# Optimization experiments

Measured on AMD Instinct MI355X. Metric: run time of the kernel, lower is better.

## Reference

```python
import jax, jax.numpy as jnp
import numpy as np

EMBED_DIM = 256
NUM_EMBEDDINGS = 1024
COMMITMENT_COST = 0.25


def setup_inputs() -> dict:
    key = jax.random.key(0)
    k1, k2 = jax.random.split(key)
    z_e = jax.random.normal(k1, (64, 32, 32, EMBED_DIM), dtype=jnp.float32)
    # variance_scaling(fan_in, uniform) ~ U(-sqrt(3/fan_in), sqrt(3/fan_in))
    lim = float(np.sqrt(3.0 / EMBED_DIM))
    codebook = jax.random.uniform(k2, (NUM_EMBEDDINGS, EMBED_DIM), dtype=jnp.float32,
                                  minval=-lim, maxval=lim)
    return {"z_e": z_e, "codebook": codebook}


def reference(z_e, codebook):
    codebook = jnp.asarray(codebook, dtype=jnp.float32)
    z_flat = jnp.reshape(z_e, (-1, codebook.shape[1]))  # [N, D]
    # ||z||^2 - 2 z.c + ||c||^2 -> [N, K]
    distances = (jnp.sum(z_flat ** 2, axis=1, keepdims=True)
                 - 2.0 * jnp.dot(z_flat, codebook.T)
                 + jnp.sum(codebook ** 2, axis=1))
    encoding_indices = jnp.argmin(distances, axis=1)  # [N]
    quantized = jnp.reshape(codebook[encoding_indices], z_e.shape)
    commitment_loss = COMMITMENT_COST * jnp.mean((jax.lax.stop_gradient(quantized) - z_e) ** 2)
    embedding_loss = jnp.mean((quantized - jax.lax.stop_gradient(z_e)) ** 2)
    quantized = z_e + jax.lax.stop_gradient(quantized - z_e)  # straight-through
    return (quantized, commitment_loss, embedding_loss, encoding_indices)
```

## Files before the change

kernel.cpp:

```cpp
#include <hip/hip_runtime.h>

#define NROWS  65536
#define DIM    256
#define KCB    1024
#define DELTA  0.012f
#define DELTA2 2.0e-4f

typedef __attribute__((ext_vector_type(8))) _Float16 v8h;
typedef __attribute__((ext_vector_type(4))) float v4f;
typedef __attribute__((ext_vector_type(4))) int   v4i;

__device__ __forceinline__ unsigned short h16(float x) {
  _Float16 h = (_Float16)x;
  return __builtin_bit_cast(unsigned short, h);
}
__device__ __forceinline__ unsigned pk2h(float a, float b) {
  return (unsigned)h16(a) | ((unsigned)h16(b) << 16);
}
__device__ __forceinline__ v4i pk8h(float4 a, float4 b) {
  v4i r; r.x = (int)pk2h(a.x,a.y); r.y = (int)pk2h(a.z,a.w);
  r.z = (int)pk2h(b.x,b.y); r.w = (int)pk2h(b.z,b.w);
  return r;
}
__device__ __forceinline__ float f16f(float x) { return (float)(_Float16)x; }
__device__ __forceinline__ void gld16(const void* g, void* l) {
  __builtin_amdgcn_global_load_lds(
      (const __attribute__((address_space(1))) unsigned int*)g,
      (__attribute__((address_space(3))) unsigned int*)l, 16, 0, 0);
}

__global__ __launch_bounds__(256) void prep_kernel(const float* __restrict__ cb,
                                                   float* __restrict__ cnorm,
                                                   unsigned short* __restrict__ cbh,
                                                   unsigned short* __restrict__ cbl,
                                                   int* __restrict__ cnt,
                                                   int* __restrict__ cnt2) {
  int g = blockIdx.x * 256 + threadIdx.x;
  if (g == 0) { *cnt = 0; *cnt2 = 0; }
  int k = g >> 2, q = g & 3;
  int nt = k >> 7, c = k & 127;
  const float4* row = reinterpret_cast<const float4*>(cb + (size_t)k * DIM) + q * 16;
  size_t off = (size_t)((nt * 4 + q) * 128 + c) * 64;
  unsigned short* dh = cbh + off;
  unsigned short* dl = cbl + off;
  int xr = (c & 7) << 3;
  double s = 0.0;
#pragma unroll
  for (int i = 0; i < 8; ++i) {
    float4 a = row[2 * i], b = row[2 * i + 1];
    s += (double)a.x * a.x + (double)a.y * a.y + (double)a.z * a.z + (double)a.w * a.w;
    s += (double)b.x * b.x + (double)b.y * b.y + (double)b.z * b.z + (double)b.w * b.w;
    *(v4i*)(dh + ((i * 8) ^ xr)) = pk8h(a, b);
    float4 ar, br;
    ar.x = a.x - f16f(a.x); ar.y = a.y - f16f(a.y);
    ar.z = a.z - f16f(a.z); ar.w = a.w - f16f(a.w);
    br.x = b.x - f16f(b.x); br.y = b.y - f16f(b.y);
    br.z = b.z - f16f(b.z); br.w = b.w - f16f(b.w);
    *(v4i*)(dl + ((i * 8) ^ xr)) = pk8h(ar, br);
  }
  s += __shfl_xor(s, 1);
  s += __shfl_xor(s, 2);
  if (q == 0) cnorm[k] = (float)s;
}

__global__ __launch_bounds__(256, 2) void vq_mfma(
    const float* __restrict__ z, const unsigned short* __restrict__ cbh,
    const float* __restrict__ cnw, int* __restrict__ idx_arr,
    int* __restrict__ list, int* __restrict__ cnt) {
  __shared__ __align__(16) short S[32768];

  const int t = threadIdx.x;
  const int l = t & 63;
  const int w = t >> 6;
  const int l15 = l & 15, lhi = l >> 4;
  const int wm = w * 32;
  const int r0 = blockIdx.x * 128;

#pragma unroll
  for (int p = 0; p < 16; ++p) {
    int u = t + p * 256;
    int row = u >> 5, k8 = u & 31;
    const float4* s = (const float4*)(z + (size_t)(r0 + row) * DIM + k8 * 8);
    float4 a = s[0], b = s[1];
    *(v4i*)(S + row * 256 + ((k8 * 8) ^ ((row & 7) << 3))) = pk8h(a, b);
  }
  __syncthreads();

  v8h A[2][8];
#pragma unroll
  for (int mf = 0; mf < 2; ++mf) {
    int arow = wm + mf * 16 + l15;
    int base = arow * 256, xr = (arow & 7) << 3;
#pragma unroll
    for (int ks8 = 0; ks8 < 8; ++ks8)
      A[mf][ks8] = *(const v8h*)(S + base + ((ks8 * 32 + lhi * 8) ^ xr));
  }
  __syncthreads();

  auto stageC = [&](int p) {
    const char* gb = (const char*)cbh + (size_t)p * 32768 + w * 8192 + l * 16;
    char* lb = (char*)(S + (p & 1) * 16384) + w * 8192;
#pragma unroll
    for (int j = 0; j < 8; ++j) gld16(gb + j * 1024, lb + j * 1024);
  };

  int bcode[8], boff[8], bxr[8];
#pragma unroll
  for (int nf = 0; nf < 8; ++nf) {
    bcode[nf] = nf * 16 + l15;
    boff[nf] = bcode[nf] * 64;
    bxr[nf] = (bcode[nf] & 7) << 3;
  }

  float m1[8], m2[8]; int i1[8];
#pragma unroll
  for (int sl = 0; sl < 8; ++sl) { m1[sl] = 3.0e38f; m2[sl] = 3.0e38f; i1[sl] = 0; }

  stageC(0);
  __syncthreads();

  for (int nt = 0; nt < 8; ++nt) {
    float cnv[8];
#pragma unroll
    for (int nf = 0; nf < 8; ++nf) cnv[nf] = cnw[nt * 128 + bcode[nf]];

    v4f acc[2][8];
#pragma unroll
    for (int mf = 0; mf < 2; ++mf)
#pragma unroll
      for (int nf = 0; nf < 8; ++nf) acc[mf][nf] = (v4f){0.f, 0.f, 0.f, 0.f};

    for (int kh = 0; kh < 2; ++kh) {
      int p = nt * 2 + kh;
      if (p < 15) stageC(p + 1);
      const short* cur = S + (p & 1) * 16384;
#pragma unroll
      for (int ks = 0; ks < 4; ++ks) {
        int sub = (ks >> 1) * 8192;
        int ko = (ks & 1) * 32 + lhi * 8;
        v8h b[8];
#pragma unroll
        for (int nf = 0; nf < 8; ++nf)
          b[nf] = *(const v8h*)(cur + sub + boff[nf] + (ko ^ bxr[nf]));
#pragma unroll
        for (int mf = 0; mf < 2; ++mf)
#pragma unroll
          for (int nf = 0; nf < 8; ++nf)
            acc[mf][nf] = __builtin_amdgcn_mfma_f32_16x16x32_f16(A[mf][kh * 4 + ks], b[nf], acc[mf][nf], 0, 0, 0);
      }
      __syncthreads();
    }

#pragma unroll
    for (int mf = 0; mf < 2; ++mf)
#pragma unroll
      for (int nf = 0; nf < 8; ++nf) {
        int code = nt * 128 + bcode[nf];
#pragma unroll
        for (int r = 0; r < 4; ++r) {
          float s = fmaf(-2.f, acc[mf][nf][r], cnv[nf]);
          int sl = mf * 4 + r;
          m2[sl] = fminf(m2[sl], fmaxf(m1[sl], s));
          bool lt = s < m1[sl];
          i1[sl] = lt ? code : i1[sl];
          m1[sl] = lt ? s : m1[sl];
        }
      }
  }

#pragma unroll
  for (int off = 1; off < 16; off <<= 1) {
#pragma unroll
    for (int sl = 0; sl < 8; ++sl) {
      float o1 = __shfl_xor(m1[sl], off);
      int   oi = __shfl_xor(i1[sl], off);
      float o2 = __shfl_xor(m2[sl], off);
      bool bb = (o1 < m1[sl]) || (o1 == m1[sl] && oi < i1[sl]);
      float hi = fmaxf(m1[sl], o1);
      m2[sl] = fminf(hi, fminf(m2[sl], o2));
      m1[sl] = bb ? o1 : m1[sl];
      i1[sl] = bb ? oi : i1[sl];
    }
  }

  if (l15 == 0) {
#pragma unroll
    for (int sl = 0; sl < 8; ++sl) {
      int row = wm + (sl >> 2) * 16 + lhi * 4 + (sl & 3);
      idx_arr[r0 + row] = i1[sl];
      if (m2[sl] - m1[sl] < DELTA) {
        int p = atomicAdd(cnt, 1);
        list[p] = r0 + row;
      }
    }
  }
}

__global__ __launch_bounds__(256, 2) void vq_refine(
    const float* __restrict__ z,
    const unsigned short* __restrict__ cbh, const unsigned short* __restrict__ cbl,
    const float* __restrict__ cnw, const int* __restrict__ list,
    const int* __restrict__ cnt, int* __restrict__ idx_arr,
    int* __restrict__ list2, int* __restrict__ cnt2) {
  __shared__ __align__(16) short Ch[2][128 * 64];
  __shared__ __align__(16) short Cl[2][128 * 64];
  __shared__ int rows_s[64];

  const int t = threadIdx.x;
  const int l = t & 63, w = t >> 6;
  const int l15 = l & 15, lhi = l >> 4;
  const int n = *cnt;
  const int ngroups = (n + 63) >> 6;

  auto stage2 = [&](int g, int buf) {
    size_t go = (size_t)g * 16384 + w * 4096 + l * 16;
    char* lh = (char*)Ch[buf] + w * 4096;
    char* ll = (char*)Cl[buf] + w * 4096;
#pragma unroll
    for (int j = 0; j < 4; ++j) gld16((const char*)cbh + go + j * 1024, lh + j * 1024);
#pragma unroll
    for (int j = 0; j < 4; ++j) gld16((const char*)cbl + go + j * 1024, ll + j * 1024);
  };

  const int bxr = (l15 & 7) << 3;

  for (int grp = blockIdx.x; grp < ngroups; grp += gridDim.x) {
    int base = grp * 64;
    __syncthreads();
    if (t < 64) rows_s[t] = list[min(base + t, n - 1)];
    __syncthreads();
    int rowg = rows_s[w * 16 + l15];

    v8h Ah[8], Al[8];
#pragma unroll
    for (int ks8 = 0; ks8 < 8; ++ks8) {
      const float* p = z + (size_t)rowg * 256 + ks8 * 32 + lhi * 8;
      float4 a = *(const float4*)p, b = *(const float4*)(p + 4);
      v8h hv, lv;
      hv[0] = (_Float16)a.x; lv[0] = (_Float16)(a.x - (float)hv[0]);
      hv[1] = (_Float16)a.y; lv[1] = (_Float16)(a.y - (float)hv[1]);
      hv[2] = (_Float16)a.z; lv[2] = (_Float16)(a.z - (float)hv[2]);
      hv[3] = (_Float16)a.w; lv[3] = (_Float16)(a.w - (float)hv[3]);
      hv[4] = (_Float16)b.x; lv[4] = (_Float16)(b.x - (float)hv[4]);
      hv[5] = (_Float16)b.y; lv[5] = (_Float16)(b.y - (float)hv[5]);
      hv[6] = (_Float16)b.z; lv[6] = (_Float16)(b.z - (float)hv[6]);
      hv[7] = (_Float16)b.w; lv[7] = (_Float16)(b.w - (float)hv[7]);
      Ah[ks8] = hv; Al[ks8] = lv;
    }

    stage2(0, 0);
    __syncthreads();

    float m1[4], m2[4]; int i1[4];
#pragma unroll
    for (int r = 0; r < 4; ++r) { m1[r] = 3.0e38f; m2[r] = 3.0e38f; i1[r] = 0; }

    for (int nt = 0; nt < 8; ++nt) {
      float cnv[8];
#pragma unroll
      for (int nf = 0; nf < 8; ++nf) cnv[nf] = cnw[nt * 128 + nf * 16 + l15];

      v4f acc[8];
#pragma unroll
      for (int nf = 0; nf < 8; ++nf) acc[nf] = (v4f){0.f, 0.f, 0.f, 0.f};

      for (int kc = 0; kc < 4; ++kc) {
        int g = nt * 4 + kc;
        if (g < 31) stage2(g + 1, (g + 1) & 1);
        const short* ch = Ch[g & 1];
        const short* cl = Cl[g & 1];
#pragma unroll
        for (int ks = 0; ks < 2; ++ks) {
          int ko = (ks * 32 + lhi * 8) ^ bxr;
          v8h bh[8], bl[8];
#pragma unroll
          for (int nf = 0; nf < 8; ++nf) {
            int bo = (nf * 16 + l15) * 64 + ko;
            bh[nf] = *(const v8h*)(ch + bo);
            bl[nf] = *(const v8h*)(cl + bo);
          }
          v8h ah = Ah[kc * 2 + ks], al = Al[kc * 2 + ks];
#pragma unroll
          for (int nf = 0; nf < 8; ++nf) {
            acc[nf] = __builtin_amdgcn_mfma_f32_16x16x32_f16(al, bh[nf], acc[nf], 0, 0, 0);
            acc[nf] = __builtin_amdgcn_mfma_f32_16x16x32_f16(ah, bl[nf], acc[nf], 0, 0, 0);
            acc[nf] = __builtin_amdgcn_mfma_f32_16x16x32_f16(ah, bh[nf], acc[nf], 0, 0, 0);
          }
        }
        __syncthreads();
      }

#pragma unroll
      for (int nf = 0; nf < 8; ++nf) {
        int code = nt * 128 + nf * 16 + l15;
#pragma unroll
        for (int r = 0; r < 4; ++r) {
          float s = fmaf(-2.f, acc[nf][r], cnv[nf]);
          m2[r] = fminf(m2[r], fmaxf(m1[r], s));
          bool lt = s < m1[r];
          i1[r] = lt ? code : i1[r];
          m1[r] = lt ? s : m1[r];
        }
      }
    }

#pragma unroll
    for (int off = 1; off < 16; off <<= 1) {
#pragma unroll
      for (int r = 0; r < 4; ++r) {
        float o1 = __shfl_xor(m1[r], off);
        int   oi = __shfl_xor(i1[r], off);
        float o2 = __shfl_xor(m2[r], off);
        bool bb = (o1 < m1[r]) || (o1 == m1[r] && oi < i1[r]);
        float hi = fmaxf(m1[r], o1);
        m2[r] = fminf(hi, fminf(m2[r], o2));
        m1[r] = bb ? o1 : m1[r];
        i1[r] = bb ? oi : i1[r];
      }
    }

    if (l15 == 0) {
#pragma unroll
      for (int r = 0; r < 4; ++r) {
        int fr = w * 16 + lhi * 4 + r;
        if (base + fr < n) {
          int grow = rows_s[fr];
          idx_arr[grow] = i1[r];
          if (m2[r] - m1[r] < DELTA2) {
            int p = atomicAdd(cnt2, 1);
            list2[p] = grow;
          }
        }
      }
    }
  }
}

__global__ __launch_bounds__(256) void vq_rescue(
    const float* __restrict__ z, const float* __restrict__ cb,
    const float* __restrict__ cnw, const int* __restrict__ list,
    const int* __restrict__ cnt, int* __restrict__ idx_arr) {
  __shared__ float zs[256];
  __shared__ float As;
  __shared__ float wmin[4];
  __shared__ int   widx[4];

  const int t = threadIdx.x;
  const int l = t & 63, w = t >> 6;
  const int n = *cnt;

  for (int i = blockIdx.x; i < n; i += gridDim.x) {
    int row = list[i];
    __syncthreads();
    if (t < 64) ((float4*)zs)[t] = ((const float4*)(z + (size_t)row * DIM))[t];
    __syncthreads();
    if (t < 4) {
      double s = 0.0;
      const float* zz = zs + t * 64;
      for (int d = 0; d < 64; ++d) { float v = zz[d]; s += (double)v * v; }
      s += __shfl_xor(s, 1);
      s += __shfl_xor(s, 2);
      if (t == 0) As = (float)s;
    }
    __syncthreads();
    float Af = As;

    const float4* c0 = (const float4*)(cb + (size_t)(t      ) * DIM);
    const float4* c1 = (const float4*)(cb + (size_t)(t + 256) * DIM);
    const float4* c2 = (const float4*)(cb + (size_t)(t + 512) * DIM);
    const float4* c3 = (const float4*)(cb + (size_t)(t + 768) * DIM);
    float a0 = 0.f, a1 = 0.f, a2 = 0.f, a3 = 0.f;
    for (int d4 = 0; d4 < 64; ++d4) {
      float4 zq = *(const float4*)(zs + d4 * 4);
      float4 va = c0[d4], vb = c1[d4], vc = c2[d4], vd = c3[d4];
      a0 = fmaf(zq.x, va.x, a0); a0 = fmaf(zq.y, va.y, a0);
      a0 = fmaf(zq.z, va.z, a0); a0 = fmaf(zq.w, va.w, a0);
      a1 = fmaf(zq.x, vb.x, a1); a1 = fmaf(zq.y, vb.y, a1);
      a1 = fmaf(zq.z, vb.z, a1); a1 = fmaf(zq.w, vb.w, a1);
      a2 = fmaf(zq.x, vc.x, a2); a2 = fmaf(zq.y, vc.y, a2);
      a2 = fmaf(zq.z, vc.z, a2); a2 = fmaf(zq.w, vc.w, a2);
      a3 = fmaf(zq.x, vd.x, a3); a3 = fmaf(zq.y, vd.y, a3);
      a3 = fmaf(zq.z, vd.z, a3); a3 = fmaf(zq.w, vd.w, a3);
    }
    float accs[4] = {a0, a1, a2, a3};
    float mv = 3.0e38f; int mi = 0;
#pragma unroll
    for (int j = 0; j < 4; ++j) {
      int code = t + j * 256;
      float t1 = fmaf(-2.f, accs[j], Af);
      float t2 = t1 + cnw[code];
      if (t2 < mv) { mv = t2; mi = code; }
    }
#pragma unroll
    for (int off = 1; off < 64; off <<= 1) {
      float ov = __shfl_xor(mv, off);
      int   oi = __shfl_xor(mi, off);
      if (ov < mv || (ov == mv && oi < mi)) { mv = ov; mi = oi; }
    }
    if (l == 0) { wmin[w] = mv; widx[w] = mi; }
    __syncthreads();
    if (t == 0) {
      float bm = wmin[0]; int bi = widx[0];
#pragma unroll
      for (int q = 1; q < 4; ++q)
        if (wmin[q] < bm || (wmin[q] == bm && widx[q] < bi)) { bm = wmin[q]; bi = widx[q]; }
      idx_arr[row] = bi;
    }
    __syncthreads();
  }
}

__global__ __launch_bounds__(256) void vq_epilogue(
    const float* __restrict__ z, const float* __restrict__ cb,
    const int* __restrict__ idx_arr, float* __restrict__ out_q,
    float* __restrict__ out_idx, double* __restrict__ partial) {
  __shared__ int idxs[16];
  __shared__ double lw[4];
  const int t = threadIdx.x;
  const int b0 = blockIdx.x * 16;
  if (t < 16) {
    int k = idx_arr[b0 + t];
    idxs[t] = k;
    out_idx[b0 + t] = (float)k;
  }
  __syncthreads();
  const float4* zb = (const float4*)(z + (size_t)b0 * DIM);
  float4* qb = (float4*)(out_q + (size_t)b0 * DIM);
  double ls = 0.0;
#pragma unroll
  for (int p = 0; p < 4; ++p) {
    int fi = p * 256 + t;
    int ki = idxs[fi >> 6];
    float4 zv = zb[fi];
    float4 cv = ((const float4*)(cb + (size_t)ki * DIM))[fi & 63];
    float dx = cv.x - zv.x, dy = cv.y - zv.y, dz = cv.z - zv.z, dw = cv.w - zv.w;
    float4 o; o.x = zv.x + dx; o.y = zv.y + dy; o.z = zv.z + dz; o.w = zv.w + dw;
    qb[fi] = o;
    ls += (double)dx * dx + (double)dy * dy + (double)dz * dz + (double)dw * dw;
  }
#pragma unroll
  for (int off = 1; off < 64; off <<= 1) ls += __shfl_xor(ls, off);
  if ((t & 63) == 0) lw[t >> 6] = ls;
  __syncthreads();
  if (t == 0) partial[blockIdx.x] = lw[0] + lw[1] + lw[2] + lw[3];
}

__global__ __launch_bounds__(256) void finalize_kernel(const double* __restrict__ partial,
                                                       float* __restrict__ out_losses) {
  __shared__ double lw[4];
  const int t = threadIdx.x;
  double s = 0.0;
  for (int i = t; i < 4096; i += 256) s += partial[i];
#pragma unroll
  for (int off = 1; off < 64; off <<= 1) s += __shfl_xor(s, off);
  if ((t & 63) == 0) lw[t >> 6] = s;
  __syncthreads();
  if (t == 0) {
    double mse = (lw[0] + lw[1] + lw[2] + lw[3]) / ((double)NROWS * (double)DIM);
    out_losses[0] = (float)(0.25 * mse);
    out_losses[1] = (float)mse;
  }
}

extern "C" void kernel_launch(void* const* d_in, const int* in_sizes, int n_in,
                              void* d_out, int out_size, void* d_ws, size_t ws_size,
                              hipStream_t stream) {
  const float* z  = (const float*)d_in[0];
  const float* cb = (const float*)d_in[1];
  float* out = (float*)d_out;

  char* ws = (char*)d_ws;
  int*            cnt     = (int*)(ws + 0);
  int*            cnt2    = (int*)(ws + 8);
  float*          cnorm   = (float*)(ws + 4096);
  double*         partial = (double*)(ws + 8192);
  int*            idx_arr = (int*)(ws + 40960);
  int*            list    = (int*)(ws + 303104);
  int*            list2   = (int*)(ws + 565248);
  unsigned short* cbh     = (unsigned short*)(ws + 827392);
  unsigned short* cbl     = (unsigned short*)(ws + 1351680);

  float* out_q      = out;
  float* out_losses = out + 16777216;
  float* out_idx    = out + 16777218;

  prep_kernel<<<16, 256, 0, stream>>>(cb, cnorm, cbh, cbl, cnt, cnt2);
  vq_mfma<<<NROWS / 128, 256, 0, stream>>>(z, cbh, cnorm, idx_arr, list, cnt);
  vq_refine<<<256, 256, 0, stream>>>(z, cbh, cbl, cnorm, list, cnt, idx_arr, list2, cnt2);
  vq_rescue<<<256, 256, 0, stream>>>(z, cb, cnorm, list2, cnt2, idx_arr);
  vq_epilogue<<<NROWS / 16, 256, 0, stream>>>(z, cb, idx_arr, out_q, out_idx, partial);
  finalize_kernel<<<1, 256, 0, stream>>>(partial, out_losses);
}
```

Baseline: 170.2 us.

## Fuse epilogue into MFMA kernel, triple-buffer codebook staging, patch refined rows

Measured after the change: 324.2 us. +90.4%, slower.

```diff
diff --git a/kernel.cpp b/kernel.cpp
--- a/kernel.cpp
+++ b/kernel.cpp
@@ -65,13 +65,16 @@
 
 __global__ __launch_bounds__(256, 2) void vq_mfma(
     const float* __restrict__ z, const unsigned short* __restrict__ cbh,
-    const float* __restrict__ cnw, int* __restrict__ idx_arr,
-    int* __restrict__ list, int* __restrict__ cnt) {
+    const float* __restrict__ cnw, const float* __restrict__ cb,
+    int* __restrict__ idx_arr, int* __restrict__ list, int* __restrict__ cnt,
+    float* __restrict__ out_q, float* __restrict__ out_idx,
+    float* __restrict__ rowloss) {
   __shared__ __align__(16) short S[32768];
+  __shared__ float CNS[1024];
+  __shared__ int idxs2[128];
 
   const int t = threadIdx.x;
-  const int l = t & 63;
-  const int w = t >> 6;
+  const int l = t & 63, w = t >> 6;
   const int l15 = l & 15, lhi = l >> 4;
   const int wm = w * 32;
   const int r0 = blockIdx.x * 128;
@@ -84,6 +87,8 @@
     float4 a = s[0], b = s[1];
     *(v4i*)(S + row * 256 + ((k8 * 8) ^ ((row & 7) << 3))) = pk8h(a, b);
   }
+#pragma unroll
+  for (int j = 0; j < 4; ++j) CNS[t + j * 256] = cnw[t + j * 256];
   __syncthreads();
 
   v8h A[2][8];
@@ -97,11 +102,11 @@
   }
   __syncthreads();
 
-  auto stageC = [&](int p) {
-    const char* gb = (const char*)cbh + (size_t)p * 32768 + w * 8192 + l * 16;
-    char* lb = (char*)(S + (p & 1) * 16384) + w * 8192;
-#pragma unroll
-    for (int j = 0; j < 8; ++j) gld16(gb + j * 1024, lb + j * 1024);
+  auto stageC = [&](int g) {
+    const char* gb = (const char*)cbh + (size_t)g * 16384 + w * 4096 + l * 16;
+    char* lb = (char*)S + (g % 3) * 16384 + w * 4096 + l * 16;
+#pragma unroll
+    for (int j = 0; j < 4; ++j) gld16(gb + j * 1024, lb + j * 1024);
   };
 
   int bcode[8], boff[8], bxr[8];
@@ -116,56 +121,54 @@
 #pragma unroll
   for (int sl = 0; sl < 8; ++sl) { m1[sl] = 3.0e38f; m2[sl] = 3.0e38f; i1[sl] = 0; }
 
-  stageC(0);
-  __syncthreads();
-
-  for (int nt = 0; nt < 8; ++nt) {
-    float cnv[8];
-#pragma unroll
-    for (int nf = 0; nf < 8; ++nf) cnv[nf] = cnw[nt * 128 + bcode[nf]];
-
-    v4f acc[2][8];
-#pragma unroll
-    for (int mf = 0; mf < 2; ++mf)
-#pragma unroll
-      for (int nf = 0; nf < 8; ++nf) acc[mf][nf] = (v4f){0.f, 0.f, 0.f, 0.f};
-
-    for (int kh = 0; kh < 2; ++kh) {
-      int p = nt * 2 + kh;
-      if (p < 15) stageC(p + 1);
-      const short* cur = S + (p & 1) * 16384;
-#pragma unroll
-      for (int ks = 0; ks < 4; ++ks) {
-        int sub = (ks >> 1) * 8192;
-        int ko = (ks & 1) * 32 + lhi * 8;
-        v8h b[8];
+  v4f acc[2][8];
+
+  stageC(0); stageC(1);
+  for (int g = 0; g < 32; ++g) {
+    if (g < 31) asm volatile("s_waitcnt vmcnt(4)" ::: "memory");
+    else        asm volatile("s_waitcnt vmcnt(0)" ::: "memory");
+    __builtin_amdgcn_s_barrier();
+    __builtin_amdgcn_sched_barrier(0);
+    if (g + 2 < 32) stageC(g + 2);
+    const int kc = g & 3;
+    if (kc == 0) {
+#pragma unroll
+      for (int mf = 0; mf < 2; ++mf)
+#pragma unroll
+        for (int nf = 0; nf < 8; ++nf) acc[mf][nf] = (v4f){0.f, 0.f, 0.f, 0.f};
+    }
+    const short* cur = S + (g % 3) * 8192;
+#pragma unroll
+    for (int ks = 0; ks < 2; ++ks) {
+      v8h b[8];
+#pragma unroll
+      for (int nf = 0; nf < 8; ++nf)
+        b[nf] = *(const v8h*)(cur + boff[nf] + ((ks * 32 + lhi * 8) ^ bxr[nf]));
+#pragma unroll
+      for (int mf = 0; mf < 2; ++mf)
 #pragma unroll
         for (int nf = 0; nf < 8; ++nf)
-          b[nf] = *(const v8h*)(cur + sub + boff[nf] + (ko ^ bxr[nf]));
-#pragma unroll
-        for (int mf = 0; mf < 2; ++mf)
-#pragma unroll
-          for (int nf = 0; nf < 8; ++nf)
-            acc[mf][nf] = __builtin_amdgcn_mfma_f32_16x16x32_f16(A[mf][kh * 4 + ks], b[nf], acc[mf][nf], 0, 0, 0);
-      }
-      __syncthreads();
-    }
-
-#pragma unroll
-    for (int mf = 0; mf < 2; ++mf)
-#pragma unroll
-      for (int nf = 0; nf < 8; ++nf) {
-        int code = nt * 128 + bcode[nf];
-#pragma unroll
-        for (int r = 0; r < 4; ++r) {
-          float s = fmaf(-2.f, acc[mf][nf][r], cnv[nf]);
-          int sl = mf * 4 + r;
-          m2[sl] = fminf(m2[sl], fmaxf(m1[sl], s));
-          bool lt = s < m1[sl];
-          i1[sl] = lt ? code : i1[sl];
-          m1[sl] = lt ? s : m1[sl];
+          acc[mf][nf] = __builtin_amdgcn_mfma_f32_16x16x32_f16(A[mf][kc * 2 + ks], b[nf], acc[mf][nf], 0, 0, 0);
+    }
+    if (kc == 3) {
+      int nt = g >> 2;
+#pragma unroll
+      for (int mf = 0; mf < 2; ++mf)
+#pragma unroll
+        for (int nf = 0; nf < 8; ++nf) {
+          int code = nt * 128 + bcode[nf];
+          float cn = CNS[nt * 128 + bcode[nf]];
+#pragma unroll
+          for (int r = 0; r < 4; ++r) {
+            float s = fmaf(-2.f, acc[mf][nf][r], cn);
+            int sl = mf * 4 + r;
+            m2[sl] = __builtin_amdgcn_fmed3f(s, m1[sl], m2[sl]);
+            bool lt = s < m1[sl];
+            i1[sl] = lt ? code : i1[sl];
+            m1[sl] = lt ? s : m1[sl];
+          }
         }
-      }
+    }
   }
 
 #pragma unroll
@@ -188,48 +191,46 @@
     for (int sl = 0; sl < 8; ++sl) {
       int row = wm + (sl >> 2) * 16 + lhi * 4 + (sl & 3);
       idx_arr[r0 + row] = i1[sl];
+      out_idx[r0 + row] = (float)i1[sl];
+      idxs2[row] = i1[sl];
       if (m2[sl] - m1[sl] < DELTA) {
         int p = atomicAdd(cnt, 1);
         list[p] = r0 + row;
       }
     }
   }
-}
-
-__global__ __launch_bounds__(256, 2) void vq_refine(
+  __syncthreads();
+
+  for (int p = 0; p < 32; ++p) {
+    int row = p * 4 + w;
+    int k = idxs2[row];
+    float4 zv = ((const float4*)(z + (size_t)(r0 + row) * DIM))[l];
+    float4 cv = ((const float4*)(cb + (size_t)k * DIM))[l];
+    float dx = cv.x - zv.x, dy = cv.y - zv.y, dz = cv.z - zv.z, dw = cv.w - zv.w;
+    float4 o; o.x = zv.x + dx; o.y = zv.y + dy; o.z = zv.z + dz; o.w = zv.w + dw;
+    ((float4*)(out_q + (size_t)(r0 + row) * DIM))[l] = o;
+    double ls = (double)dx * dx + (double)dy * dy + (double)dz * dz + (double)dw * dw;
+#pragma unroll
+    for (int off = 1; off < 64; off <<= 1) ls += __shfl_xor(ls, off);
+    if (l == 0) rowloss[r0 + row] = (float)ls;
+  }
+}
+
+__global__ __launch_bounds__(64) void vq_refine(
     const float* __restrict__ z,
     const unsigned short* __restrict__ cbh, const unsigned short* __restrict__ cbl,
     const float* __restrict__ cnw, const int* __restrict__ list,
     const int* __restrict__ cnt, int* __restrict__ idx_arr,
     int* __restrict__ list2, int* __restrict__ cnt2) {
-  __shared__ __align__(16) short Ch[2][128 * 64];
-  __shared__ __align__(16) short Cl[2][128 * 64];
-  __shared__ int rows_s[64];
-
-  const int t = threadIdx.x;
-  const int l = t & 63, w = t >> 6;
+  const int l = threadIdx.x;
   const int l15 = l & 15, lhi = l >> 4;
   const int n = *cnt;
-  const int ngroups = (n + 63) >> 6;
-
-  auto stage2 = [&](int g, int buf) {
-    size_t go = (size_t)g * 16384 + w * 4096 + l * 16;
-    char* lh = (char*)Ch[buf] + w * 4096;
-    char* ll = (char*)Cl[buf] + w * 4096;
-#pragma unroll
-    for (int j = 0; j < 4; ++j) gld16((const char*)cbh + go + j * 1024, lh + j * 1024);
-#pragma unroll
-    for (int j = 0; j < 4; ++j) gld16((const char*)cbl + go + j * 1024, ll + j * 1024);
-  };
-
+  const int ng = (n + 15) >> 4;
   const int bxr = (l15 & 7) << 3;
 
-  for (int grp = blockIdx.x; grp < ngroups; grp += gridDim.x) {
-    int base = grp * 64;
-    __syncthreads();
-    if (t < 64) rows_s[t] = list[min(base + t, n - 1)];
-    __syncthreads();
-    int rowg = rows_s[w * 16 + l15];
+  for (int grp = blockIdx.x; grp < ng; grp += gridDim.x) {
+    const int base = grp * 16;
+    int rowg = list[min(base + l15, n - 1)];
 
     v8h Ah[8], Al[8];
 #pragma unroll
@@ -248,9 +249,6 @@
       Ah[ks8] = hv; Al[ks8] = lv;
     }
 
-    stage2(0, 0);
-    __syncthreads();
-
     float m1[4], m2[4]; int i1[4];
 #pragma unroll
     for (int r = 0; r < 4; ++r) { m1[r] = 3.0e38f; m2[r] = 3.0e38f; i1[r] = 0; }
@@ -266,28 +264,24 @@
 
       for (int kc = 0; kc < 4; ++kc) {
         int g = nt * 4 + kc;
-        if (g < 31) stage2(g + 1, (g + 1) & 1);
-        const short* ch = Ch[g & 1];
-        const short* cl = Cl[g & 1];
 #pragma unroll
         for (int ks = 0; ks < 2; ++ks) {
           int ko = (ks * 32 + lhi * 8) ^ bxr;
-          v8h bh[8], bl[8];
+          v8h bh[8], bl8[8];
 #pragma unroll
           for (int nf = 0; nf < 8; ++nf) {
-            int bo = (nf * 16 + l15) * 64 + ko;
-            bh[nf] = *(const v8h*)(ch + bo);
-            bl[nf] = *(const v8h*)(cl + bo);
+            size_t bo = (size_t)g * 8192 + (size_t)(nf * 16 + l15) * 64 + ko;
+            bh[nf]  = *(const v8h*)(cbh + bo);
+            bl8[nf] = *(const v8h*)(cbl + bo);
           }
           v8h ah = Ah[kc * 2 + ks], al = Al[kc * 2 + ks];
 #pragma unroll
           for (int nf = 0; nf < 8; ++nf) {
             acc[nf] = __builtin_amdgcn_mfma_f32_16x16x32_f16(al, bh[nf], acc[nf], 0, 0, 0);
-            acc[nf] = __builtin_amdgcn_mfma_f32_16x16x32_f16(ah, bl[nf], acc[nf], 0, 0, 0);
+            acc[nf] = __builtin_amdgcn_mfma_f32_16x16x32_f16(ah, bl8[nf], acc[nf], 0, 0, 0);
             acc[nf] = __builtin_amdgcn_mfma_f32_16x16x32_f16(ah, bh[nf], acc[nf], 0, 0, 0);
           }
         }
-        __syncthreads();
       }
 
 #pragma unroll
@@ -296,7 +290,7 @@
 #pragma unroll
         for (int r = 0; r < 4; ++r) {
           float s = fmaf(-2.f, acc[nf][r], cnv[nf]);
-          m2[r] = fminf(m2[r], fmaxf(m1[r], s));
+          m2[r] = __builtin_amdgcn_fmed3f(s, m1[r], m2[r]);
           bool lt = s < m1[r];
           i1[r] = lt ? code : i1[r];
           m1[r] = lt ? s : m1[r];
@@ -322,9 +316,9 @@
     if (l15 == 0) {
 #pragma unroll
       for (int r = 0; r < 4; ++r) {
-        int fr = w * 16 + lhi * 4 + r;
+        int fr = lhi * 4 + r;
         if (base + fr < n) {
-          int grow = rows_s[fr];
+          int grow = list[base + fr];
           idx_arr[grow] = i1[r];
           if (m2[r] - m1[r] < DELTA2) {
             int p = atomicAdd(cnt2, 1);
@@ -410,47 +404,34 @@
   }
 }
 
-__global__ __launch_bounds__(256) void vq_epilogue(
+__global__ __launch_bounds__(64) void vq_patch(
     const float* __restrict__ z, const float* __restrict__ cb,
+    const int* __restrict__ list, const int* __restrict__ cnt,
     const int* __restrict__ idx_arr, float* __restrict__ out_q,
-    float* __restrict__ out_idx, double* __restrict__ partial) {
-  __shared__ int idxs[16];
-  __shared__ double lw[4];
-  const int t = threadIdx.x;
-  const int b0 = blockIdx.x * 16;
-  if (t < 16) {
-    int k = idx_arr[b0 + t];
-    idxs[t] = k;
-    out_idx[b0 + t] = (float)k;
-  }
-  __syncthreads();
-  const float4* zb = (const float4*)(z + (size_t)b0 * DIM);
-  float4* qb = (float4*)(out_q + (size_t)b0 * DIM);
-  double ls = 0.0;
-#pragma unroll
-  for (int p = 0; p < 4; ++p) {
-    int fi = p * 256 + t;
-    int ki = idxs[fi >> 6];
-    float4 zv = zb[fi];
-    float4 cv = ((const float4*)(cb + (size_t)ki * DIM))[fi & 63];
+    float* __restrict__ out_idx, float* __restrict__ rowloss) {
+  const int l = threadIdx.x;
+  const int n = *cnt;
+  for (int i = blockIdx.x; i < n; i += gridDim.x) {
+    int row = list[i];
+    int k = idx_arr[row];
+    float4 zv = ((const float4*)(z + (size_t)row * DIM))[l];
+    float4 cv = ((const float4*)(cb + (size_t)k * DIM))[l];
     float dx = cv.x - zv.x, dy = cv.y - zv.y, dz = cv.z - zv.z, dw = cv.w - zv.w;
     float4 o; o.x = zv.x + dx; o.y = zv.y + dy; o.z = zv.z + dz; o.w = zv.w + dw;
-    qb[fi] = o;
-    ls += (double)dx * dx + (double)dy * dy + (double)dz * dz + (double)dw * dw;
-  }
-#pragma unroll
-  for (int off = 1; off < 64; off <<= 1) ls += __shfl_xor(ls, off);
-  if ((t & 63) == 0) lw[t >> 6] = ls;
-  __syncthreads();
-  if (t == 0) partial[blockIdx.x] = lw[0] + lw[1] + lw[2] + lw[3];
-}
-
-__global__ __launch_bounds__(256) void finalize_kernel(const double* __restrict__ partial,
+    ((float4*)(out_q + (size_t)row * DIM))[l] = o;
+    double ls = (double)dx * dx + (double)dy * dy + (double)dz * dz + (double)dw * dw;
+#pragma unroll
+    for (int off = 1; off < 64; off <<= 1) ls += __shfl_xor(ls, off);
+    if (l == 0) { rowloss[row] = (float)ls; out_idx[row] = (float)k; }
+  }
+}
+
+__global__ __launch_bounds__(256) void finalize_kernel(const float* __restrict__ rowloss,
                                                        float* __restrict__ out_losses) {
   __shared__ double lw[4];
   const int t = threadIdx.x;
   double s = 0.0;
-  for (int i = t; i < 4096; i += 256) s += partial[i];
+  for (int i = t; i < NROWS; i += 256) s += (double)rowloss[i];
 #pragma unroll
   for (int off = 1; off < 64; off <<= 1) s += __shfl_xor(s, off);
   if ((t & 63) == 0) lw[t >> 6] = s;
@@ -473,21 +454,22 @@
   int*            cnt     = (int*)(ws + 0);
   int*            cnt2    = (int*)(ws + 8);
   float*          cnorm   = (float*)(ws + 4096);
-  double*         partial = (double*)(ws + 8192);
-  int*            idx_arr = (int*)(ws + 40960);
-  int*            list    = (int*)(ws + 303104);
-  int*            list2   = (int*)(ws + 565248);
-  unsigned short* cbh     = (unsigned short*)(ws + 827392);
-  unsigned short* cbl     = (unsigned short*)(ws + 1351680);
+  float*          rowloss = (float*)(ws + 8192);
+  int*            idx_arr = (int*)(ws + 270336);
+  int*            list    = (int*)(ws + 532480);
+  int*            list2   = (int*)(ws + 794624);
+  unsigned short* cbh     = (unsigned short*)(ws + 1056768);
+  unsigned short* cbl     = (unsigned short*)(ws + 1581056);
 
   float* out_q      = out;
   float* out_losses = out + 16777216;
   float* out_idx    = out + 16777218;
 
   prep_kernel<<<16, 256, 0, stream>>>(cb, cnorm, cbh, cbl, cnt, cnt2);
-  vq_mfma<<<NROWS / 128, 256, 0, stream>>>(z, cbh, cnorm, idx_arr, list, cnt);
-  vq_refine<<<256, 256, 0, stream>>>(z, cbh, cbl, cnorm, list, cnt, idx_arr, list2, cnt2);
+  vq_mfma<<<NROWS / 128, 256, 0, stream>>>(z, cbh, cnorm, cb, idx_arr, list, cnt,
+                                           out_q, out_idx, rowloss);
+  vq_refine<<<1024, 64, 0, stream>>>(z, cbh, cbl, cnorm, list, cnt, idx_arr, list2, cnt2);
   vq_rescue<<<256, 256, 0, stream>>>(z, cb, cnorm, list2, cnt2, idx_arr);
-  vq_epilogue<<<NROWS / 16, 256, 0, stream>>>(z, cb, idx_arr, out_q, out_idx, partial);
-  finalize_kernel<<<1, 256, 0, stream>>>(partial, out_losses);
-}
+  vq_patch<<<1024, 64, 0, stream>>>(z, cb, list, cnt, idx_arr, out_q, out_idx, rowloss);
+  finalize_kernel<<<1, 256, 0, stream>>>(rowloss, out_losses);
+}
```

## Halve LDS footprint in vq_mfma to raise occupancy to four blocks per CU

Applied to the files above, without the earlier changes.

Result: slower. 289.1 us (+69.8%).

```diff
diff --git a/kernel.cpp b/kernel.cpp
--- a/kernel.cpp
+++ b/kernel.cpp
@@ -63,45 +63,49 @@
   if (q == 0) cnorm[k] = (float)s;
 }
 
-__global__ __launch_bounds__(256, 2) void vq_mfma(
+__global__ __launch_bounds__(256, 4) void vq_mfma(
     const float* __restrict__ z, const unsigned short* __restrict__ cbh,
     const float* __restrict__ cnw, int* __restrict__ idx_arr,
     int* __restrict__ list, int* __restrict__ cnt) {
-  __shared__ __align__(16) short S[32768];
+  __shared__ __align__(16) short S[16384];
 
   const int t = threadIdx.x;
-  const int l = t & 63;
-  const int w = t >> 6;
+  const int l = t & 63, w = t >> 6;
   const int l15 = l & 15, lhi = l >> 4;
   const int wm = w * 32;
   const int r0 = blockIdx.x * 128;
 
-#pragma unroll
-  for (int p = 0; p < 16; ++p) {
-    int u = t + p * 256;
-    int row = u >> 5, k8 = u & 31;
-    const float4* s = (const float4*)(z + (size_t)(r0 + row) * DIM + k8 * 8);
-    float4 a = s[0], b = s[1];
-    *(v4i*)(S + row * 256 + ((k8 * 8) ^ ((row & 7) << 3))) = pk8h(a, b);
-  }
-  __syncthreads();
-
   v8h A[2][8];
-#pragma unroll
-  for (int mf = 0; mf < 2; ++mf) {
-    int arow = wm + mf * 16 + l15;
-    int base = arow * 256, xr = (arow & 7) << 3;
-#pragma unroll
-    for (int ks8 = 0; ks8 < 8; ++ks8)
-      A[mf][ks8] = *(const v8h*)(S + base + ((ks8 * 32 + lhi * 8) ^ xr));
-  }
-  __syncthreads();
-
-  auto stageC = [&](int p) {
-    const char* gb = (const char*)cbh + (size_t)p * 32768 + w * 8192 + l * 16;
-    char* lb = (char*)(S + (p & 1) * 16384) + w * 8192;
-#pragma unroll
-    for (int j = 0; j < 8; ++j) gld16(gb + j * 1024, lb + j * 1024);
+
+#pragma unroll
+  for (int h = 0; h < 2; ++h) {
+#pragma unroll
+    for (int p = 0; p < 8; ++p) {
+      int u = t + p * 256;
+      int rl = u >> 5, k8 = u & 31;
+      const float4* s = (const float4*)(z + (size_t)(r0 + h * 64 + rl) * DIM + k8 * 8);
+      float4 a = s[0], b = s[1];
+      *(v4i*)(S + rl * 256 + ((k8 * 8) ^ ((rl & 7) << 3))) = pk8h(a, b);
+    }
+    __syncthreads();
+    if ((w >> 1) == h) {
+#pragma unroll
+      for (int mf = 0; mf < 2; ++mf) {
+        int arow = wm + mf * 16 + l15 - h * 64;
+        int base = arow * 256, xr = (arow & 7) << 3;
+#pragma unroll
+        for (int ks8 = 0; ks8 < 8; ++ks8)
+          A[mf][ks8] = *(const v8h*)(S + base + ((ks8 * 32 + lhi * 8) ^ xr));
+      }
+    }
+    __syncthreads();
+  }
+
+  auto stageC = [&](int g) {
+    const char* gb = (const char*)cbh + (size_t)g * 16384 + w * 4096 + l * 16;
+    char* lb = (char*)S + (g & 1) * 16384 + w * 4096 + l * 16;
+#pragma unroll
+    for (int j = 0; j < 4; ++j) gld16(gb + j * 1024, lb + j * 1024);
   };
 
   int bcode[8], boff[8], bxr[8];
@@ -116,56 +120,53 @@
 #pragma unroll
   for (int sl = 0; sl < 8; ++sl) { m1[sl] = 3.0e38f; m2[sl] = 3.0e38f; i1[sl] = 0; }
 
+  v4f acc[2][8];
+
   stageC(0);
   __syncthreads();
 
-  for (int nt = 0; nt < 8; ++nt) {
-    float cnv[8];
-#pragma unroll
-    for (int nf = 0; nf < 8; ++nf) cnv[nf] = cnw[nt * 128 + bcode[nf]];
-
-    v4f acc[2][8];
-#pragma unroll
-    for (int mf = 0; mf < 2; ++mf)
-#pragma unroll
-      for (int nf = 0; nf < 8; ++nf) acc[mf][nf] = (v4f){0.f, 0.f, 0.f, 0.f};
-
-    for (int kh = 0; kh < 2; ++kh) {
-      int p = nt * 2 + kh;
-      if (p < 15) stageC(p + 1);
-      const short* cur = S + (p & 1) * 16384;
-#pragma unroll
-      for (int ks = 0; ks < 4; ++ks) {
-        int sub = (ks >> 1) * 8192;
-        int ko = (ks & 1) * 32 + lhi * 8;
-        v8h b[8];
+  for (int g = 0; g < 32; ++g) {
+    if (g < 31) stageC(g + 1);
+    const int kc = g & 3;
+    if (kc == 0) {
+#pragma unroll
+      for (int mf = 0; mf < 2; ++mf)
+#pragma unroll
+        for (int nf = 0; nf < 8; ++nf) acc[mf][nf] = (v4f){0.f, 0.f, 0.f, 0.f};
+    }
+    const short* cur = S + (g & 1) * 8192;
+#pragma unroll
+    for (int ks = 0; ks < 2; ++ks) {
+      v8h b[8];
+#pragma unroll
+      for (int nf = 0; nf < 8; ++nf)
+        b[nf] = *(const v8h*)(cur + boff[nf] + ((ks * 32 + lhi * 8) ^ bxr[nf]));
+#pragma unroll
+      for (int mf = 0; mf < 2; ++mf)
 #pragma unroll
         for (int nf = 0; nf < 8; ++nf)
-          b[nf] = *(const v8h*)(cur + sub + boff[nf] + (ko ^ bxr[nf]));
-#pragma unroll
-        for (int mf = 0; mf < 2; ++mf)
-#pragma unroll
-          for (int nf = 0; nf < 8; ++nf)
-            acc[mf][nf] = __builtin_amdgcn_mfma_f32_16x16x32_f16(A[mf][kh * 4 + ks], b[nf], acc[mf][nf], 0, 0, 0);
-      }
-      __syncthreads();
-    }
-
-#pragma unroll
-    for (int mf = 0; mf < 2; ++mf)
-#pragma unroll
-      for (int nf = 0; nf < 8; ++nf) {
-        int code = nt * 128 + bcode[nf];
-#pragma unroll
-        for (int r = 0; r < 4; ++r) {
-          float s = fmaf(-2.f, acc[mf][nf][r], cnv[nf]);
-          int sl = mf * 4 + r;
-          m2[sl] = fminf(m2[sl], fmaxf(m1[sl], s));
-          bool lt = s < m1[sl];
-          i1[sl] = lt ? code : i1[sl];
-          m1[sl] = lt ? s : m1[sl];
+          acc[mf][nf] = __builtin_amdgcn_mfma_f32_16x16x32_f16(A[mf][kc * 2 + ks], b[nf], acc[mf][nf], 0, 0, 0);
+    }
+    if (kc == 3) {
+      int nt = g >> 2;
+#pragma unroll
+      for (int mf = 0; mf < 2; ++mf)
+#pragma unroll
+        for (int nf = 0; nf < 8; ++nf) {
+          int code = nt * 128 + bcode[nf];
+          float cn = cnw[nt * 128 + bcode[nf]];
+#pragma unroll
+          for (int r = 0; r < 4; ++r) {
+            float s = fmaf(-2.f, acc[mf][nf][r], cn);
+            int sl = mf * 4 + r;
+            m2[sl] = __builtin_amdgcn_fmed3f(s, m1[sl], m2[sl]);
+            bool lt = s < m1[sl];
+            i1[sl] = lt ? code : i1[sl];
+            m1[sl] = lt ? s : m1[sl];
+          }
         }
-      }
+    }
+    __syncthreads();
   }
 
 #pragma unroll
@@ -217,9 +218,9 @@
     char* lh = (char*)Ch[buf] + w * 4096;
     char* ll = (char*)Cl[buf] + w * 4096;
 #pragma unroll
-    for (int j = 0; j < 4; ++j) gld16((const char*)cbh + go + j * 1024, lh + j * 1024);
-#pragma unroll
-    for (int j = 0; j < 4; ++j) gld16((const char*)cbl + go + j * 1024, ll + j * 1024);
+    for (int j = 0; j < 4; ++j) gld16((const char*)cbh + go + j * 1024, lh + l * 16 + j * 1024);
+#pragma unroll
+    for (int j = 0; j < 4; ++j) gld16((const char*)cbl + go + j * 1024, ll + l * 16 + j * 1024);
   };
 
   const int bxr = (l15 & 7) << 3;
@@ -272,18 +273,18 @@
 #pragma unroll
         for (int ks = 0; ks < 2; ++ks) {
           int ko = (ks * 32 + lhi * 8) ^ bxr;
-          v8h bh[8], bl[8];
+          v8h bh[8], bl8[8];
 #pragma unroll
           for (int nf = 0; nf < 8; ++nf) {
             int bo = (nf * 16 + l15) * 64 + ko;
-            bh[nf] = *(const v8h*)(ch + bo);
-            bl[nf] = *(const v8h*)(cl + bo);
+            bh[nf]  = *(const v8h*)(ch + bo);
+            bl8[nf] = *(const v8h*)(cl + bo);
           }
           v8h ah = Ah[kc * 2 + ks], al = Al[kc * 2 + ks];
 #pragma unroll
           for (int nf = 0; nf < 8; ++nf) {
             acc[nf] = __builtin_amdgcn_mfma_f32_16x16x32_f16(al, bh[nf], acc[nf], 0, 0, 0);
-            acc[nf] = __builtin_amdgcn_mfma_f32_16x16x32_f16(ah, bl[nf], acc[nf], 0, 0, 0);
+            acc[nf] = __builtin_amdgcn_mfma_f32_16x16x32_f16(ah, bl8[nf], acc[nf], 0, 0, 0);
             acc[nf] = __builtin_amdgcn_mfma_f32_16x16x32_f16(ah, bh[nf], acc[nf], 0, 0, 0);
           }
         }
@@ -296,7 +297,7 @@
 #pragma unroll
         for (int r = 0; r < 4; ++r) {
           float s = fmaf(-2.f, acc[nf][r], cnv[nf]);
-          m2[r] = fminf(m2[r], fmaxf(m1[r], s));
+          m2[r] = __builtin_amdgcn_fmed3f(s, m1[r], m2[r]);
           bool lt = s < m1[r];
           i1[r] = lt ? code : i1[r];
           m1[r] = lt ? s : m1[r];
```

## Split refine kernel across codebook quarters and merge partial top-2 results

Applied to the files above, without the earlier changes.

Measured after the change: 166.8 us. -2.0%, faster.

```diff
diff --git a/kernel.cpp b/kernel.cpp
--- a/kernel.cpp
+++ b/kernel.cpp
@@ -5,6 +5,7 @@
 #define KCB    1024
 #define DELTA  0.012f
 #define DELTA2 2.0e-4f
+#define NRMAX  65536
 
 typedef __attribute__((ext_vector_type(8))) _Float16 v8h;
 typedef __attribute__((ext_vector_type(4))) float v4f;
@@ -200,10 +201,10 @@
     const float* __restrict__ z,
     const unsigned short* __restrict__ cbh, const unsigned short* __restrict__ cbl,
     const float* __restrict__ cnw, const int* __restrict__ list,
-    const int* __restrict__ cnt, int* __restrict__ idx_arr,
-    int* __restrict__ list2, int* __restrict__ cnt2) {
-  __shared__ __align__(16) short Ch[2][128 * 64];
-  __shared__ __align__(16) short Cl[2][128 * 64];
+    const int* __restrict__ cnt,
+    float* __restrict__ pm1, float* __restrict__ pm2, int* __restrict__ pi1) {
+  __shared__ __align__(16) short Ch[2][8192];
+  __shared__ __align__(16) short Cl[2][8192];
   __shared__ int rows_s[64];
 
   const int t = threadIdx.x;
@@ -211,6 +212,7 @@
   const int l15 = l & 15, lhi = l >> 4;
   const int n = *cnt;
   const int ngroups = (n + 63) >> 6;
+  const int cq = blockIdx.x & 3;
 
   auto stage2 = [&](int g, int buf) {
     size_t go = (size_t)g * 16384 + w * 4096 + l * 16;
@@ -224,7 +226,7 @@
 
   const int bxr = (l15 & 7) << 3;
 
-  for (int grp = blockIdx.x; grp < ngroups; grp += gridDim.x) {
+  for (int grp = blockIdx.x >> 2; grp < ngroups; grp += (gridDim.x >> 2)) {
     int base = grp * 64;
     __syncthreads();
     if (t < 64) rows_s[t] = list[min(base + t, n - 1)];
@@ -248,14 +250,16 @@
       Ah[ks8] = hv; Al[ks8] = lv;
     }
 
-    stage2(0, 0);
+    stage2(cq * 8, 0);
     __syncthreads();
 
     float m1[4], m2[4]; int i1[4];
 #pragma unroll
     for (int r = 0; r < 4; ++r) { m1[r] = 3.0e38f; m2[r] = 3.0e38f; i1[r] = 0; }
 
-    for (int nt = 0; nt < 8; ++nt) {
+#pragma unroll
+    for (int tnt = 0; tnt < 2; ++tnt) {
+      int nt = cq * 2 + tnt;
       float cnv[8];
 #pragma unroll
       for (int nf = 0; nf < 8; ++nf) cnv[nf] = cnw[nt * 128 + nf * 16 + l15];
@@ -265,25 +269,26 @@
       for (int nf = 0; nf < 8; ++nf) acc[nf] = (v4f){0.f, 0.f, 0.f, 0.f};
 
       for (int kc = 0; kc < 4; ++kc) {
+        int ph = tnt * 4 + kc;
         int g = nt * 4 + kc;
-        if (g < 31) stage2(g + 1, (g + 1) & 1);
-        const short* ch = Ch[g & 1];
-        const short* cl = Cl[g & 1];
+        if (ph < 7) stage2(g + 1, (ph + 1) & 1);
+        const short* ch = Ch[ph & 1];
+        const short* cl = Cl[ph & 1];
 #pragma unroll
         for (int ks = 0; ks < 2; ++ks) {
           int ko = (ks * 32 + lhi * 8) ^ bxr;
-          v8h bh[8], bl[8];
+          v8h bh[8], bl8[8];
 #pragma unroll
           for (int nf = 0; nf < 8; ++nf) {
             int bo = (nf * 16 + l15) * 64 + ko;
-            bh[nf] = *(const v8h*)(ch + bo);
-            bl[nf] = *(const v8h*)(cl + bo);
+            bh[nf]  = *(const v8h*)(ch + bo);
+            bl8[nf] = *(const v8h*)(cl + bo);
           }
           v8h ah = Ah[kc * 2 + ks], al = Al[kc * 2 + ks];
 #pragma unroll
           for (int nf = 0; nf < 8; ++nf) {
             acc[nf] = __builtin_amdgcn_mfma_f32_16x16x32_f16(al, bh[nf], acc[nf], 0, 0, 0);
-            acc[nf] = __builtin_amdgcn_mfma_f32_16x16x32_f16(ah, bl[nf], acc[nf], 0, 0, 0);
+            acc[nf] = __builtin_amdgcn_mfma_f32_16x16x32_f16(ah, bl8[nf], acc[nf], 0, 0, 0);
             acc[nf] = __builtin_amdgcn_mfma_f32_16x16x32_f16(ah, bh[nf], acc[nf], 0, 0, 0);
           }
         }
@@ -323,16 +328,43 @@
 #pragma unroll
       for (int r = 0; r < 4; ++r) {
         int fr = w * 16 + lhi * 4 + r;
-        if (base + fr < n) {
-          int grow = rows_s[fr];
-          idx_arr[grow] = i1[r];
-          if (m2[r] - m1[r] < DELTA2) {
-            int p = atomicAdd(cnt2, 1);
-            list2[p] = grow;
-          }
+        int pos = base + fr;
+        if (pos < n) {
+          pm1[cq * NRMAX + pos] = m1[r];
+          pm2[cq * NRMAX + pos] = m2[r];
+          pi1[cq * NRMAX + pos] = i1[r];
         }
       }
     }
+  }
+}
+
+__global__ __launch_bounds__(256) void vq_merge(
+    const int* __restrict__ list, const int* __restrict__ cnt,
+    const float* __restrict__ pm1, const float* __restrict__ pm2,
+    const int* __restrict__ pi1, int* __restrict__ idx_arr,
+    int* __restrict__ list2, int* __restrict__ cnt2) {
+  int i = blockIdx.x * 256 + threadIdx.x;
+  int n = *cnt;
+  if (i >= n) return;
+  float m1 = pm1[i], m2 = pm2[i];
+  int   i1 = pi1[i];
+#pragma unroll
+  for (int cq = 1; cq < 4; ++cq) {
+    float o1 = pm1[cq * NRMAX + i];
+    float o2 = pm2[cq * NRMAX + i];
+    int   oi = pi1[cq * NRMAX + i];
+    bool bb = (o1 < m1) || (o1 == m1 && oi < i1);
+    float hi = fmaxf(m1, o1);
+    m2 = fminf(hi, fminf(m2, o2));
+    m1 = bb ? o1 : m1;
+    i1 = bb ? oi : i1;
+  }
+  int row = list[i];
+  idx_arr[row] = i1;
+  if (m2 - m1 < DELTA2) {
+    int p = atomicAdd(cnt2, 1);
+    list2[p] = row;
   }
 }
 
@@ -479,6 +511,9 @@
   int*            list2   = (int*)(ws + 565248);
   unsigned short* cbh     = (unsigned short*)(ws + 827392);
   unsigned short* cbl     = (unsigned short*)(ws + 1351680);
+  float*          pm1     = (float*)(ws + 1875968);
+  float*          pm2     = (float*)(ws + 2924544);
+  int*            pi1     = (int*)(ws + 3973120);
 
   float* out_q      = out;
   float* out_losses = out + 16777216;
@@ -486,7 +521,8 @@
 
   prep_kernel<<<16, 256, 0, stream>>>(cb, cnorm, cbh, cbl, cnt, cnt2);
   vq_mfma<<<NROWS / 128, 256, 0, stream>>>(z, cbh, cnorm, idx_arr, list, cnt);
-  vq_refine<<<256, 256, 0, stream>>>(z, cbh, cbl, cnorm, list, cnt, idx_arr, list2, cnt2);
+  vq_refine<<<1024, 256, 0, stream>>>(z, cbh, cbl, cnorm, list, cnt, pm1, pm2, pi1);
+  vq_merge<<<NRMAX / 256, 256, 0, stream>>>(list, cnt, pm1, pm2, pi1, idx_arr, list2, cnt2);
   vq_rescue<<<256, 256, 0, stream>>>(z, cb, cnorm, list2, cnt2, idx_arr);
   vq_epilogue<<<NROWS / 16, 256, 0, stream>>>(z, cb, idx_arr, out_q, out_idx, partial);
   finalize_kernel<<<1, 256, 0, stream>>>(partial, out_losses);
```
